# Kernel optimization log

Measured on AMD Instinct MI355X. Metric: run time of the kernel, lower is better.

The kernel has to match this reference:

```python
import jax, jax.numpy as jnp
import numpy as np

ITERS = 3          # num_iterations
EPS_ATTN = 1e-8    # epsilon offset on attention
LN_EPS = 1e-5      # torch LayerNorm default eps


def _ln(x, g, b):
    m = x.mean(-1, keepdims=True)
    v = ((x - m) ** 2).mean(-1, keepdims=True)
    return (x - m) * jax.lax.rsqrt(v + LN_EPS) * g + b


def setup_inputs() -> dict:
    key = jax.random.key(0)
    ks = jax.random.split(key, 16)
    B, N, D, S, H = 64, 4096, 64, 8, 128

    def lin_w(k, fan_in, fan_out):
        lim = (1.0 / fan_in) ** 0.5
        return jax.random.uniform(k, (fan_in, fan_out), minval=-lim, maxval=lim, dtype=jnp.float32)

    def lin_b(k, fan_in, fan_out):
        lim = (1.0 / fan_in) ** 0.5
        return jax.random.uniform(k, (fan_out,), minval=-lim, maxval=lim, dtype=jnp.float32)

    return {
        "inputs": jax.random.normal(ks[0], (B, N, D), dtype=jnp.float32),
        "noise": jax.random.normal(ks[1], (B, S, D), dtype=jnp.float32),
        "slots_mu": jax.random.normal(ks[2], (1, 1, D), dtype=jnp.float32),
        "slots_log_sigma": jax.random.uniform(ks[3], (1, 1, D), minval=-0.3, maxval=0.3, dtype=jnp.float32),
        "wq": lin_w(ks[4], D, D), "bq": lin_b(ks[4], D, D),
        "wk": lin_w(ks[5], D, D), "bk": lin_b(ks[5], D, D),
        "wv": lin_w(ks[6], D, D), "bv": lin_b(ks[6], D, D),
        "w_ih": lin_w(ks[7], D, 3 * D), "b_ih": lin_b(ks[7], D, 3 * D),
        "w_hh": lin_w(ks[8], D, 3 * D), "b_hh": lin_b(ks[8], D, 3 * D),
        "w1": lin_w(ks[9], D, H), "b1": lin_b(ks[9], D, H),
        "w2": lin_w(ks[10], H, D), "b2": lin_b(ks[10], H, D),
        "g_in": jnp.ones((D,), jnp.float32), "beta_in": jnp.zeros((D,), jnp.float32),
        "g_sl": jnp.ones((D,), jnp.float32), "beta_sl": jnp.zeros((D,), jnp.float32),
        "g_ff": jnp.ones((D,), jnp.float32), "beta_ff": jnp.zeros((D,), jnp.float32),
    }


def reference(inputs, noise, slots_mu, slots_log_sigma, wq, bq, wk, bk, wv, bv,
              w_ih, b_ih, w_hh, b_hh, w1, b1, w2, b2,
              g_in, beta_in, g_sl, beta_sl, g_ff, beta_ff):
    b, n, d = inputs.shape
    scale = d ** -0.5

    slots = slots_mu + jnp.exp(slots_log_sigma) * noise          # [b, S, d]
    x = _ln(inputs, g_in, beta_in)
    k = x @ wk + bk                                              # [b, n, d]
    v = x @ wv + bv                                              # [b, n, d]

    for _ in range(ITERS):
        slots_prev = slots
        q = _ln(slots, g_sl, beta_sl) @ wq + bq                  # [b, S, d]
        dots = jnp.einsum('bid,bjd->bij', q, k) * scale          # [b, S, n]
        attn = jax.nn.softmax(dots, axis=1) + EPS_ATTN           # softmax over slots
        attn = attn / attn.sum(-1, keepdims=True)                # renorm over inputs
        updates = jnp.einsum('bjd,bij->bid', v, attn)            # [b, S, d]

        # GRUCell (torch gate order: reset, update, new)
        gx = updates @ w_ih + b_ih
        gh = slots_prev @ w_hh + b_hh
        xr, xz, xn = jnp.split(gx, 3, axis=-1)
        hr, hz, hn = jnp.split(gh, 3, axis=-1)
        r = jax.nn.sigmoid(xr + hr)
        z = jax.nn.sigmoid(xz + hz)
        nw = jnp.tanh(xn + r * hn)
        slots = (1.0 - z) * nw + z * slots_prev

        # residual MLP
        ff = _ln(slots, g_ff, beta_ff)
        slots = slots + (jax.nn.relu(ff @ w1 + b1) @ w2 + b2)
    return slots
```

## Files before the change

### kernel.cpp

```cpp
#include <hip/hip_runtime.h>
#include <math.h>

#define LN_EPS 1e-5f
#define EPS_ATTN 1e-8f
#define SCALE 0.125f
#define CHUNKS 16

__device__ __forceinline__ float wsum64(float v) {
#pragma unroll
  for (int m = 1; m <= 32; m <<= 1) v += __shfl_xor(v, m, 64);
  return v;
}

__device__ __forceinline__ float red16(float v) {
  v += __int_as_float(__builtin_amdgcn_update_dpp(0, __float_as_int(v), 0xB1, 0xF, 0xF, true));
  v += __int_as_float(__builtin_amdgcn_update_dpp(0, __float_as_int(v), 0x4E, 0xF, 0xF, true));
  v += __int_as_float(__builtin_amdgcn_update_dpp(0, __float_as_int(v), 0x124, 0xF, 0xF, true));
  v += __int_as_float(__builtin_amdgcn_update_dpp(0, __float_as_int(v), 0x128, 0xF, 0xF, true));
  return v;
}

__device__ void slot_qk_wave(int bi, float o, int lane,
    const float* __restrict__ M, const float* __restrict__ cvec,
    const float* __restrict__ uvec, const float* __restrict__ s0v,
    const float* __restrict__ g_sl, const float* __restrict__ beta_sl,
    float* __restrict__ qk, float* __restrict__ qb)
{
  float s  = wsum64(o);
  float s2 = wsum64(o * o);
  float mean = s * (1.0f / 64.0f);
  float var  = s2 * (1.0f / 64.0f) - mean * mean;
  float rstd = rsqrtf(var + LN_EPS);
  float ln = (o - mean) * rstd * g_sl[lane] + beta_sl[lane];

  float qv = cvec[lane];
#pragma unroll
  for (int t = 0; t < 64; ++t) qv += __shfl(ln, t, 64) * M[t * 64 + lane];
  qk[bi * 64 + lane] = qv;
  float pb = wsum64(ln * uvec[lane]);
  if (lane == 0) qb[bi] = s0v[0] + pb;
}

__device__ void slot_update_wave(int bi, int lane, int do_next,
    const float* __restrict__ S_in, float* __restrict__ S_out,
    float* __restrict__ acc, float* __restrict__ asum,
    const float* __restrict__ wv, const float* __restrict__ bv,
    const float* __restrict__ w_ih, const float* __restrict__ b_ih,
    const float* __restrict__ w_hh, const float* __restrict__ b_hh,
    const float* __restrict__ w1, const float* __restrict__ b1,
    const float* __restrict__ w2, const float* __restrict__ b2,
    const float* __restrict__ g_ff, const float* __restrict__ beta_ff,
    const float* __restrict__ M, const float* __restrict__ cvec,
    const float* __restrict__ uvec, const float* __restrict__ s0v,
    const float* __restrict__ g_sl, const float* __restrict__ beta_sl,
    float* __restrict__ qk, float* __restrict__ qb)
{
  float asv = asum[bi];
  float av  = acc[bi * 64 + lane];
  float v   = av / asv;
  if (do_next) {
    acc[bi * 64 + lane] = 0.0f;
    if (lane == 0) asum[bi] = 0.0f;
  }
  float sp = S_in[bi * 64 + lane];

  float upd = bv[lane];
#pragma unroll
  for (int e = 0; e < 64; ++e) upd += __shfl(v, e, 64) * wv[e * 64 + lane];

  float gxr = b_ih[lane], gxz = b_ih[64 + lane], gxn = b_ih[128 + lane];
  float ghr = b_hh[lane], ghz = b_hh[64 + lane], ghn = b_hh[128 + lane];
#pragma unroll 16
  for (int e = 0; e < 64; ++e) {
    float uu = __shfl(upd, e, 64), hh = __shfl(sp, e, 64);
    const float* wi = w_ih + e * 192;
    const float* wh = w_hh + e * 192;
    gxr += uu * wi[lane]; gxz += uu * wi[64 + lane]; gxn += uu * wi[128 + lane];
    ghr += hh * wh[lane]; ghz += hh * wh[64 + lane]; ghn += hh * wh[128 + lane];
  }
  float r  = 1.0f / (1.0f + __expf(-(gxr + ghr)));
  float z  = 1.0f / (1.0f + __expf(-(gxz + ghz)));
  float nw = tanhf(gxn + r * ghn);
  float sn = (1.0f - z) * nw + z * sp;

  float s  = wsum64(sn);
  float s2 = wsum64(sn * sn);
  float mean = s * (1.0f / 64.0f);
  float var  = s2 * (1.0f / 64.0f) - mean * mean;
  float rstd = rsqrtf(var + LN_EPS);
  float ff = (sn - mean) * rstd * g_ff[lane] + beta_ff[lane];

  float h1 = b1[lane], h2 = b1[64 + lane];
#pragma unroll
  for (int e = 0; e < 64; ++e) {
    float f = __shfl(ff, e, 64);
    h1 += f * w1[e * 128 + lane];
    h2 += f * w1[e * 128 + 64 + lane];
  }
  h1 = fmaxf(h1, 0.0f);
  h2 = fmaxf(h2, 0.0f);

  float o = sn + b2[lane];
#pragma unroll
  for (int t = 0; t < 64; ++t) o += __shfl(h1, t, 64) * w2[t * 64 + lane];
#pragma unroll
  for (int t = 0; t < 64; ++t) o += __shfl(h2, t, 64) * w2[(64 + t) * 64 + lane];

  S_out[bi * 64 + lane] = o;

  if (do_next)
    slot_qk_wave(bi, o, lane, M, cvec, uvec, s0v, g_sl, beta_sl, qk, qb);
}

__global__ __launch_bounds__(64) void k_init(
    const float* __restrict__ noise, const float* __restrict__ mu,
    const float* __restrict__ lsig,
    const float* __restrict__ wq, const float* __restrict__ bq,
    const float* __restrict__ wk, const float* __restrict__ bk,
    const float* __restrict__ g_sl, const float* __restrict__ beta_sl,
    float* __restrict__ S_buf, float* __restrict__ qk, float* __restrict__ qb,
    float* __restrict__ acc, float* __restrict__ asum,
    float* __restrict__ M, float* __restrict__ cvec,
    float* __restrict__ uvec, float* __restrict__ s0v)
{
  int bi = blockIdx.x;
  int lane = threadIdx.x;
  if (bi < 512) {
    float sl = mu[lane] + __expf(lsig[lane]) * noise[bi * 64 + lane];
    S_buf[bi * 64 + lane] = sl;
    acc[bi * 64 + lane] = 0.0f;
    if (lane == 0) asum[bi] = 0.0f;

    float s  = wsum64(sl);
    float s2 = wsum64(sl * sl);
    float mean = s * (1.0f / 64.0f);
    float var  = s2 * (1.0f / 64.0f) - mean * mean;
    float rstd = rsqrtf(var + LN_EPS);
    float ln = (sl - mean) * rstd * g_sl[lane] + beta_sl[lane];

    float q = bq[lane];
#pragma unroll
    for (int t = 0; t < 64; ++t) q += __shfl(ln, t, 64) * wq[t * 64 + lane];
    float qkl = 0.0f;
#pragma unroll
    for (int d = 0; d < 64; ++d) qkl += __shfl(q, d, 64) * wk[lane * 64 + d];
    qk[bi * 64 + lane] = qkl * SCALE;
    float qbl = wsum64(q * bk[lane]);
    if (lane == 0) qb[bi] = qbl * SCALE;
  } else if (bi < 576) {
    int t = bi - 512;
    float wqv = wq[t * 64 + lane];
    float m = 0.0f;
#pragma unroll
    for (int d = 0; d < 64; ++d) m += __shfl(wqv, d, 64) * wk[lane * 64 + d];
    M[t * 64 + lane] = m * SCALE;
    float uv = wsum64(wqv * bk[lane]);
    if (lane == 0) uvec[t] = uv * SCALE;
  } else {
    float bqv = bq[lane];
    float cc = 0.0f;
#pragma unroll
    for (int j = 0; j < 64; ++j) cc += __shfl(bqv, j, 64) * wk[lane * 64 + j];
    cvec[lane] = cc * SCALE;
    float ss = wsum64(bq[lane] * bk[lane]);
    if (lane == 0) s0v[0] = ss * SCALE;
  }
}

__global__ __launch_bounds__(64) void k_update(
    const float* __restrict__ S_in, float* __restrict__ S_out,
    float* __restrict__ acc, float* __restrict__ asum,
    const float* __restrict__ wv, const float* __restrict__ bv,
    const float* __restrict__ w_ih, const float* __restrict__ b_ih,
    const float* __restrict__ w_hh, const float* __restrict__ b_hh,
    const float* __restrict__ w1, const float* __restrict__ b1,
    const float* __restrict__ w2, const float* __restrict__ b2,
    const float* __restrict__ g_ff, const float* __restrict__ beta_ff,
    const float* __restrict__ M, const float* __restrict__ cvec,
    const float* __restrict__ uvec, const float* __restrict__ s0v,
    const float* __restrict__ g_sl, const float* __restrict__ beta_sl,
    float* __restrict__ qk, float* __restrict__ qb, int do_next)
{
  slot_update_wave(blockIdx.x, threadIdx.x, do_next,
                   S_in, S_out, acc, asum, wv, bv, w_ih, b_ih, w_hh, b_hh,
                   w1, b1, w2, b2, g_ff, beta_ff, M, cvec, uvec, s0v,
                   g_sl, beta_sl, qk, qb);
}

__global__ __launch_bounds__(256) void k_main(
    const float* __restrict__ inputs,
    const float* __restrict__ g_in, const float* __restrict__ beta_in,
    const float* __restrict__ qk, const float* __restrict__ qb,
    float* __restrict__ acc, float* __restrict__ asum)
{
  __shared__ float lds_acc[4][512];
  __shared__ float lds_as[4][8];
  const int b = blockIdx.y;
  const int chunk = blockIdx.x;
  const int tid = threadIdx.x;
  const int lane = tid & 63;
  const int wave = tid >> 6;
  const int p = lane & 15;

  float4 g4  = ((const float4*)g_in)[p];
  float4 be4 = ((const float4*)beta_in)[p];
  float4 qkv[8];
  float qbv[8];
  const float4* qk4 = (const float4*)(qk + b * 512);
#pragma unroll
  for (int i = 0; i < 8; ++i) {
    qkv[i] = qk4[i * 16 + p];
    qbv[i] = qb[b * 8 + i];
  }

  float4 accl[8];
  float asl[8];
#pragma unroll
  for (int i = 0; i < 8; ++i) { accl[i] = make_float4(0.f, 0.f, 0.f, 0.f); asl[i] = 0.f; }

  const float4* in4 = (const float4*)(inputs + (size_t)b * 4096 * 64);
  const int rb0 = chunk * 256 + wave * 8;

  float4 xa = in4[rb0 * 16 + lane];
  float4 xb = in4[(rb0 + 4) * 16 + lane];
  for (int it = 0; it < 8; ++it) {
    float4 na, nb;
    if (it < 7) {
      na = in4[(rb0 + (it + 1) * 32) * 16 + lane];
      nb = in4[(rb0 + (it + 1) * 32 + 4) * 16 + lane];
    }

    {
      float s  = red16(xa.x + xa.y + xa.z + xa.w);
      float s2 = red16(xa.x * xa.x + xa.y * xa.y + xa.z * xa.z + xa.w * xa.w);
      float mean = s * 0.015625f;
      float var  = s2 * 0.015625f - mean * mean;
      float rstd = rsqrtf(var + LN_EPS);
      float4 xln;
      xln.x = (xa.x - mean) * rstd * g4.x + be4.x;
      xln.y = (xa.y - mean) * rstd * g4.y + be4.y;
      xln.z = (xa.z - mean) * rstd * g4.z + be4.z;
      xln.w = (xa.w - mean) * rstd * g4.w + be4.w;
      float dots[8];
#pragma unroll
      for (int i = 0; i < 8; ++i) {
        float d = xln.x * qkv[i].x + xln.y * qkv[i].y + xln.z * qkv[i].z + xln.w * qkv[i].w;
        dots[i] = red16(d) + qbv[i];
      }
      float pv[8];
      float ps = 0.0f;
#pragma unroll
      for (int i = 0; i < 8; ++i) { pv[i] = __expf(dots[i]); ps += pv[i]; }
      float inv = __builtin_amdgcn_rcpf(ps);
#pragma unroll
      for (int i = 0; i < 8; ++i) {
        float pp = pv[i] * inv + EPS_ATTN;
        asl[i] += pp;
        accl[i].x += pp * xln.x;
        accl[i].y += pp * xln.y;
        accl[i].z += pp * xln.z;
        accl[i].w += pp * xln.w;
      }
    }
    {
      float s  = red16(xb.x + xb.y + xb.z + xb.w);
      float s2 = red16(xb.x * xb.x + xb.y * xb.y + xb.z * xb.z + xb.w * xb.w);
      float mean = s * 0.015625f;
      float var  = s2 * 0.015625f - mean * mean;
      float rstd = rsqrtf(var + LN_EPS);
      float4 xln;
      xln.x = (xb.x - mean) * rstd * g4.x + be4.x;
      xln.y = (xb.y - mean) * rstd * g4.y + be4.y;
      xln.z = (xb.z - mean) * rstd * g4.z + be4.z;
      xln.w = (xb.w - mean) * rstd * g4.w + be4.w;
      float dots[8];
#pragma unroll
      for (int i = 0; i < 8; ++i) {
        float d = xln.x * qkv[i].x + xln.y * qkv[i].y + xln.z * qkv[i].z + xln.w * qkv[i].w;
        dots[i] = red16(d) + qbv[i];
      }
      float pv[8];
      float ps = 0.0f;
#pragma unroll
      for (int i = 0; i < 8; ++i) { pv[i] = __expf(dots[i]); ps += pv[i]; }
      float inv = __builtin_amdgcn_rcpf(ps);
#pragma unroll
      for (int i = 0; i < 8; ++i) {
        float pp = pv[i] * inv + EPS_ATTN;
        asl[i] += pp;
        accl[i].x += pp * xln.x;
        accl[i].y += pp * xln.y;
        accl[i].z += pp * xln.z;
        accl[i].w += pp * xln.w;
      }
    }
    xa = na;
    xb = nb;
  }

#pragma unroll
  for (int i = 0; i < 8; ++i) {
#pragma unroll
    for (int m = 16; m <= 32; m <<= 1) {
      accl[i].x += __shfl_xor(accl[i].x, m, 64);
      accl[i].y += __shfl_xor(accl[i].y, m, 64);
      accl[i].z += __shfl_xor(accl[i].z, m, 64);
      accl[i].w += __shfl_xor(accl[i].w, m, 64);
      asl[i]    += __shfl_xor(asl[i], m, 64);
    }
  }

  if (lane < 16) {
    float4* dst = (float4*)lds_acc[wave];
#pragma unroll
    for (int i = 0; i < 8; ++i) dst[i * 16 + p] = accl[i];
  }
  if (lane == 0) {
#pragma unroll
    for (int i = 0; i < 8; ++i) lds_as[wave][i] = asl[i];
  }
  __syncthreads();

  for (int f = tid; f < 512; f += 256) {
    float ssum = lds_acc[0][f] + lds_acc[1][f] + lds_acc[2][f] + lds_acc[3][f];
    atomicAdd(&acc[b * 512 + f], ssum);
  }
  if (tid < 8) {
    float ssum = lds_as[0][tid] + lds_as[1][tid] + lds_as[2][tid] + lds_as[3][tid];
    atomicAdd(&asum[b * 8 + tid], ssum);
  }
}

extern "C" void kernel_launch(void* const* d_in, const int* in_sizes, int n_in,
                              void* d_out, int out_size, void* d_ws, size_t ws_size,
                              hipStream_t stream) {
  const float* inputs  = (const float*)d_in[0];
  const float* noise   = (const float*)d_in[1];
  const float* mu      = (const float*)d_in[2];
  const float* lsig    = (const float*)d_in[3];
  const float* wq      = (const float*)d_in[4];
  const float* bq      = (const float*)d_in[5];
  const float* wk      = (const float*)d_in[6];
  const float* bk      = (const float*)d_in[7];
  const float* wv      = (const float*)d_in[8];
  const float* bv      = (const float*)d_in[9];
  const float* w_ih    = (const float*)d_in[10];
  const float* b_ih    = (const float*)d_in[11];
  const float* w_hh    = (const float*)d_in[12];
  const float* b_hh    = (const float*)d_in[13];
  const float* w1      = (const float*)d_in[14];
  const float* b1      = (const float*)d_in[15];
  const float* w2      = (const float*)d_in[16];
  const float* b2      = (const float*)d_in[17];
  const float* g_in    = (const float*)d_in[18];
  const float* beta_in = (const float*)d_in[19];
  const float* g_sl    = (const float*)d_in[20];
  const float* beta_sl = (const float*)d_in[21];
  const float* g_ff    = (const float*)d_in[22];
  const float* beta_ff = (const float*)d_in[23];

  float* S_buf = (float*)d_ws;
  float* qk    = S_buf + 32768;
  float* qb    = qk + 32768;
  float* acc   = qb + 512;
  float* asum  = acc + 32768;
  float* M     = asum + 512;
  float* cvec  = M + 4096;
  float* uvec  = cvec + 64;
  float* s0v   = uvec + 64;
  float* out   = (float*)d_out;

  k_init<<<577, 64, 0, stream>>>(noise, mu, lsig, wq, bq, wk, bk,
                                 g_sl, beta_sl, S_buf, qk, qb, acc, asum,
                                 M, cvec, uvec, s0v);

  for (int t = 0; t < 3; ++t) {
    k_main<<<dim3(CHUNKS, 64), 256, 0, stream>>>(inputs, g_in, beta_in,
                                                 qk, qb, acc, asum);
    float* dst = (t == 2) ? out : S_buf;
    k_update<<<512, 64, 0, stream>>>(S_buf, dst, acc, asum, wv, bv,
                                     w_ih, b_ih, w_hh, b_hh, w1, b1, w2, b2,
                                     g_ff, beta_ff, M, cvec, uvec, s0v,
                                     g_sl, beta_sl, qk, qb, (t == 2) ? 0 : 1);
  }
}
```

Before: 230.7 us.

## Stage qk in LDS, double CHUNKS, and interleave two rows for higher occupancy

Moves the per-batch qk matrix from 32 registers per thread into shared memory and sets a min-blocks-per-CU launch bound to cut register pressure and raise occupancy. It doubles the chunk count so each block handles half as many rows. The two rows' dot/exp/accumulate steps are also interleaved for more ILP. The cost is LDS reads on every row, an extra barrier, and twice as many atomic adds into the accumulators.

```diff
diff --git a/kernel.cpp b/kernel.cpp
--- a/kernel.cpp
+++ b/kernel.cpp
@@ -4,7 +4,7 @@
 #define LN_EPS 1e-5f
 #define EPS_ATTN 1e-8f
 #define SCALE 0.125f
-#define CHUNKS 16
+#define CHUNKS 32
 
 __device__ __forceinline__ float wsum64(float v) {
 #pragma unroll
@@ -167,6 +167,136 @@
   }
 }
 
+__global__ __launch_bounds__(256, 5) void k_main(
+    const float* __restrict__ inputs,
+    const float* __restrict__ g_in, const float* __restrict__ beta_in,
+    const float* __restrict__ qk, const float* __restrict__ qb,
+    float* __restrict__ acc, float* __restrict__ asum)
+{
+  __shared__ float lds_qk[512];
+  __shared__ float lds_acc[4][512];
+  __shared__ float lds_as[4][8];
+  const int b = blockIdx.y;
+  const int chunk = blockIdx.x;
+  const int tid = threadIdx.x;
+  const int lane = tid & 63;
+  const int wave = tid >> 6;
+  const int p = lane & 15;
+
+  if (tid < 128)
+    ((float4*)lds_qk)[tid] = ((const float4*)(qk + b * 512))[tid];
+
+  float4 g4  = ((const float4*)g_in)[p];
+  float4 be4 = ((const float4*)beta_in)[p];
+  float qbv[8];
+#pragma unroll
+  for (int i = 0; i < 8; ++i) qbv[i] = qb[b * 8 + i];
+
+  float4 accl[8];
+  float asl[8];
+#pragma unroll
+  for (int i = 0; i < 8; ++i) { accl[i] = make_float4(0.f, 0.f, 0.f, 0.f); asl[i] = 0.f; }
+
+  __syncthreads();
+
+  const float4* in4 = (const float4*)(inputs + (size_t)b * 4096 * 64);
+  const float4* qk4 = (const float4*)lds_qk;
+  const int rb0 = chunk * 128 + wave * 8;
+
+  float4 xa = in4[rb0 * 16 + lane];
+  float4 xb = in4[(rb0 + 4) * 16 + lane];
+  for (int it = 0; it < 4; ++it) {
+    float4 na, nb;
+    if (it < 3) {
+      na = in4[(rb0 + (it + 1) * 32) * 16 + lane];
+      nb = in4[(rb0 + (it + 1) * 32 + 4) * 16 + lane];
+    }
+
+    float sA  = red16(xa.x + xa.y + xa.z + xa.w);
+    float s2A = red16(xa.x * xa.x + xa.y * xa.y + xa.z * xa.z + xa.w * xa.w);
+    float meanA = sA * 0.015625f;
+    float varA  = s2A * 0.015625f - meanA * meanA;
+    float rstdA = rsqrtf(varA + LN_EPS);
+    float4 xlnA;
+    xlnA.x = (xa.x - meanA) * rstdA * g4.x + be4.x;
+    xlnA.y = (xa.y - meanA) * rstdA * g4.y + be4.y;
+    xlnA.z = (xa.z - meanA) * rstdA * g4.z + be4.z;
+    xlnA.w = (xa.w - meanA) * rstdA * g4.w + be4.w;
+
+    float sB  = red16(xb.x + xb.y + xb.z + xb.w);
+    float s2B = red16(xb.x * xb.x + xb.y * xb.y + xb.z * xb.z + xb.w * xb.w);
+    float meanB = sB * 0.015625f;
+    float varB  = s2B * 0.015625f - meanB * meanB;
+    float rstdB = rsqrtf(varB + LN_EPS);
+    float4 xlnB;
+    xlnB.x = (xb.x - meanB) * rstdB * g4.x + be4.x;
+    xlnB.y = (xb.y - meanB) * rstdB * g4.y + be4.y;
+    xlnB.z = (xb.z - meanB) * rstdB * g4.z + be4.z;
+    xlnB.w = (xb.w - meanB) * rstdB * g4.w + be4.w;
+
+    float pvA[8], pvB[8];
+    float psA = 0.0f, psB = 0.0f;
+#pragma unroll
+    for (int i = 0; i < 8; ++i) {
+      float4 qv = qk4[i * 16 + p];
+      float da = xlnA.x * qv.x + xlnA.y * qv.y + xlnA.z * qv.z + xlnA.w * qv.w;
+      float db = xlnB.x * qv.x + xlnB.y * qv.y + xlnB.z * qv.z + xlnB.w * qv.w;
+      da = red16(da) + qbv[i];
+      db = red16(db) + qbv[i];
+      float ea = __expf(da);
+      float eb = __expf(db);
+      pvA[i] = ea; psA += ea;
+      pvB[i] = eb; psB += eb;
+    }
+    float invA = __builtin_amdgcn_rcpf(psA);
+    float invB = __builtin_amdgcn_rcpf(psB);
+#pragma unroll
+    for (int i = 0; i < 8; ++i) {
+      float ppa = pvA[i] * invA + EPS_ATTN;
+      float ppb = pvB[i] * invB + EPS_ATTN;
+      asl[i] += ppa + ppb;
+      accl[i].x += ppa * xlnA.x; accl[i].x += ppb * xlnB.x;
+      accl[i].y += ppa * xlnA.y; accl[i].y += ppb * xlnB.y;
+      accl[i].z += ppa * xlnA.z; accl[i].z += ppb * xlnB.z;
+      accl[i].w += ppa * xlnA.w; accl[i].w += ppb * xlnB.w;
+    }
+    xa = na;
+    xb = nb;
+  }
+
+#pragma unroll
+  for (int i = 0; i < 8; ++i) {
+#pragma unroll
+    for (int m = 16; m <= 32; m <<= 1) {
+      accl[i].x += __shfl_xor(accl[i].x, m, 64);
+      accl[i].y += __shfl_xor(accl[i].y, m, 64);
+      accl[i].z += __shfl_xor(accl[i].z, m, 64);
+      accl[i].w += __shfl_xor(accl[i].w, m, 64);
+      asl[i]    += __shfl_xor(asl[i], m, 64);
+    }
+  }
+
+  if (lane < 16) {
+    float4* dst = (float4*)lds_acc[wave];
+#pragma unroll
+    for (int i = 0; i < 8; ++i) dst[i * 16 + p] = accl[i];
+  }
+  if (lane == 0) {
+#pragma unroll
+    for (int i = 0; i < 8; ++i) lds_as[wave][i] = asl[i];
+  }
+  __syncthreads();
+
+  for (int f = tid; f < 512; f += 256) {
+    float ssum = lds_acc[0][f] + lds_acc[1][f] + lds_acc[2][f] + lds_acc[3][f];
+    atomicAdd(&acc[b * 512 + f], ssum);
+  }
+  if (tid < 8) {
+    float ssum = lds_as[0][tid] + lds_as[1][tid] + lds_as[2][tid] + lds_as[3][tid];
+    atomicAdd(&asum[b * 8 + tid], ssum);
+  }
+}
+
 __global__ __launch_bounds__(64) void k_update(
     const float* __restrict__ S_in, float* __restrict__ S_out,
     float* __restrict__ acc, float* __restrict__ asum,
@@ -185,150 +315,6 @@
                    S_in, S_out, acc, asum, wv, bv, w_ih, b_ih, w_hh, b_hh,
                    w1, b1, w2, b2, g_ff, beta_ff, M, cvec, uvec, s0v,
                    g_sl, beta_sl, qk, qb);
-}
-
-__global__ __launch_bounds__(256) void k_main(
-    const float* __restrict__ inputs,
-    const float* __restrict__ g_in, const float* __restrict__ beta_in,
-    const float* __restrict__ qk, const float* __restrict__ qb,
-    float* __restrict__ acc, float* __restrict__ asum)
-{
-  __shared__ float lds_acc[4][512];
-  __shared__ float lds_as[4][8];
-  const int b = blockIdx.y;
-  const int chunk = blockIdx.x;
-  const int tid = threadIdx.x;
-  const int lane = tid & 63;
-  const int wave = tid >> 6;
-  const int p = lane & 15;
-
-  float4 g4  = ((const float4*)g_in)[p];
-  float4 be4 = ((const float4*)beta_in)[p];
-  float4 qkv[8];
-  float qbv[8];
-  const float4* qk4 = (const float4*)(qk + b * 512);
-#pragma unroll
-  for (int i = 0; i < 8; ++i) {
-    qkv[i] = qk4[i * 16 + p];
-    qbv[i] = qb[b * 8 + i];
-  }
-
-  float4 accl[8];
-  float asl[8];
-#pragma unroll
-  for (int i = 0; i < 8; ++i) { accl[i] = make_float4(0.f, 0.f, 0.f, 0.f); asl[i] = 0.f; }
-
-  const float4* in4 = (const float4*)(inputs + (size_t)b * 4096 * 64);
-  const int rb0 = chunk * 256 + wave * 8;
-
-  float4 xa = in4[rb0 * 16 + lane];
-  float4 xb = in4[(rb0 + 4) * 16 + lane];
-  for (int it = 0; it < 8; ++it) {
-    float4 na, nb;
-    if (it < 7) {
-      na = in4[(rb0 + (it + 1) * 32) * 16 + lane];
-      nb = in4[(rb0 + (it + 1) * 32 + 4) * 16 + lane];
-    }
-
-    {
-      float s  = red16(xa.x + xa.y + xa.z + xa.w);
-      float s2 = red16(xa.x * xa.x + xa.y * xa.y + xa.z * xa.z + xa.w * xa.w);
-      float mean = s * 0.015625f;
-      float var  = s2 * 0.015625f - mean * mean;
-      float rstd = rsqrtf(var + LN_EPS);
-      float4 xln;
-      xln.x = (xa.x - mean) * rstd * g4.x + be4.x;
-      xln.y = (xa.y - mean) * rstd * g4.y + be4.y;
-      xln.z = (xa.z - mean) * rstd * g4.z + be4.z;
-      xln.w = (xa.w - mean) * rstd * g4.w + be4.w;
-      float dots[8];
-#pragma unroll
-      for (int i = 0; i < 8; ++i) {
-        float d = xln.x * qkv[i].x + xln.y * qkv[i].y + xln.z * qkv[i].z + xln.w * qkv[i].w;
-        dots[i] = red16(d) + qbv[i];
-      }
-      float pv[8];
-      float ps = 0.0f;
-#pragma unroll
-      for (int i = 0; i < 8; ++i) { pv[i] = __expf(dots[i]); ps += pv[i]; }
-      float inv = __builtin_amdgcn_rcpf(ps);
-#pragma unroll
-      for (int i = 0; i < 8; ++i) {
-        float pp = pv[i] * inv + EPS_ATTN;
-        asl[i] += pp;
-        accl[i].x += pp * xln.x;
-        accl[i].y += pp * xln.y;
-        accl[i].z += pp * xln.z;
-        accl[i].w += pp * xln.w;
-      }
-    }
-    {
-      float s  = red16(xb.x + xb.y + xb.z + xb.w);
-      float s2 = red16(xb.x * xb.x + xb.y * xb.y + xb.z * xb.z + xb.w * xb.w);
-      float mean = s * 0.015625f;
-      float var  = s2 * 0.015625f - mean * mean;
-      float rstd = rsqrtf(var + LN_EPS);
-      float4 xln;
-      xln.x = (xb.x - mean) * rstd * g4.x + be4.x;
-      xln.y = (xb.y - mean) * rstd * g4.y + be4.y;
-      xln.z = (xb.z - mean) * rstd * g4.z + be4.z;
-      xln.w = (xb.w - mean) * rstd * g4.w + be4.w;
-      float dots[8];
-#pragma unroll
-      for (int i = 0; i < 8; ++i) {
-        float d = xln.x * qkv[i].x + xln.y * qkv[i].y + xln.z * qkv[i].z + xln.w * qkv[i].w;
-        dots[i] = red16(d) + qbv[i];
-      }
-      float pv[8];
-      float ps = 0.0f;
-#pragma unroll
-      for (int i = 0; i < 8; ++i) { pv[i] = __expf(dots[i]); ps += pv[i]; }
-      float inv = __builtin_amdgcn_rcpf(ps);
-#pragma unroll
-      for (int i = 0; i < 8; ++i) {
-        float pp = pv[i] * inv + EPS_ATTN;
-        asl[i] += pp;
-        accl[i].x += pp * xln.x;
-        accl[i].y += pp * xln.y;
-        accl[i].z += pp * xln.z;
-        accl[i].w += pp * xln.w;
-      }
-    }
-    xa = na;
-    xb = nb;
-  }
-
-#pragma unroll
-  for (int i = 0; i < 8; ++i) {
-#pragma unroll
-    for (int m = 16; m <= 32; m <<= 1) {
-      accl[i].x += __shfl_xor(accl[i].x, m, 64);
-      accl[i].y += __shfl_xor(accl[i].y, m, 64);
-      accl[i].z += __shfl_xor(accl[i].z, m, 64);
-      accl[i].w += __shfl_xor(accl[i].w, m, 64);
-      asl[i]    += __shfl_xor(asl[i], m, 64);
-    }
-  }
-
-  if (lane < 16) {
-    float4* dst = (float4*)lds_acc[wave];
-#pragma unroll
-    for (int i = 0; i < 8; ++i) dst[i * 16 + p] = accl[i];
-  }
-  if (lane == 0) {
-#pragma unroll
-    for (int i = 0; i < 8; ++i) lds_as[wave][i] = asl[i];
-  }
-  __syncthreads();
-
-  for (int f = tid; f < 512; f += 256) {
-    float ssum = lds_acc[0][f] + lds_acc[1][f] + lds_acc[2][f] + lds_acc[3][f];
-    atomicAdd(&acc[b * 512 + f], ssum);
-  }
-  if (tid < 8) {
-    float ssum = lds_as[0][tid] + lds_as[1][tid] + lds_as[2][tid] + lds_as[3][tid];
-    atomicAdd(&asum[b * 8 + tid], ssum);
-  }
 }
 
 extern "C" void kernel_launch(void* const* d_in, const int* in_sizes, int n_in,
```

New measurement: 295.0 us. 1.28x slower.
